# Kernel optimization log

Measured on AMD Instinct MI355X. Metric: run time of the kernel, lower is better.

## Reference

```python
import jax, jax.numpy as jnp
import numpy as np

N = 100000
E = 1600000
D = 128


def setup_inputs() -> dict:
    key = jax.random.key(0)
    ks = jax.random.split(key, 6)
    x = jax.random.normal(ks[0], (N, D), dtype=jnp.float32)
    edge_row = jax.random.randint(ks[1], (E,), 0, N)
    edge_col = jax.random.randint(ks[2], (E,), 0, N)
    edge_val = jax.random.uniform(ks[3], (E,), dtype=jnp.float32)
    # Kaiming-ish init for the MLP weights
    W1 = jax.random.normal(ks[4], (D, D), dtype=jnp.float32) * (1.0 / np.sqrt(D))
    W2 = jax.random.normal(ks[5], (D, D), dtype=jnp.float32) * (1.0 / np.sqrt(D))
    b1 = jnp.zeros((D,), dtype=jnp.float32)
    b2 = jnp.zeros((D,), dtype=jnp.float32)
    eps = jnp.zeros((1,), dtype=jnp.float32)  # GIN eps, init 0
    bias = jnp.zeros((D,), dtype=jnp.float32)
    return {"x": x, "edge_row": edge_row, "edge_col": edge_col, "edge_val": edge_val,
            "W1": W1, "b1": b1, "W2": W2, "b2": b2, "eps": eps, "bias": bias}


def reference(x, edge_row, edge_col, edge_val, W1, b1, W2, b2, eps, bias):
    # sparse adj @ x : out[i] = sum_{edges (i,j)} val * x[j]
    agg = jax.ops.segment_sum(edge_val[:, None] * x[edge_col], edge_row, num_segments=N)
    h = (1.0 + eps) * x + agg                     # eps-scaled residual, [N, D]
    h = jax.nn.relu(h @ W1 + b1)                  # MLP layer 1
    h = jax.nn.relu(h @ W2 + b2)                  # MLP layer 2
    out = jax.nn.relu(h + bias)                   # bias + final relu
    return out
```

## Files before the change

### kernel.cpp

```cpp
#include <hip/hip_runtime.h>
#include <stdint.h>


static constexpr int NN = 100000;
static constexpr int NE = 1600000;
static constexpr int NB = 196;
static constexpr int EPB = 4096;
static constexpr int PB = (NE + EPB - 1) / EPB;

typedef float f32x4 __attribute__((ext_vector_type(4)));
typedef short s16x8 __attribute__((ext_vector_type(8)));

__device__ __forceinline__ uint16_t f2bf(float f) {
  uint32_t u = __float_as_uint(f);
  u += 0x7fffu + ((u >> 16) & 1u);
  return (uint16_t)(u >> 16);
}
__device__ __forceinline__ float2 bf2f(uint32_t w) {
  float2 r;
  r.x = __uint_as_float(w << 16);
  r.y = __uint_as_float(w & 0xffff0000u);
  return r;
}

template <int WIDTH>
__device__ __forceinline__ int* scan_inc(int* s0, int* s1, int tid) {
  int* pin = s0;
  int* pout = s1;
  for (int off = 1; off < WIDTH; off <<= 1) {
    if (tid < WIDTH) pout[tid] = pin[tid] + ((tid >= off) ? pin[tid - off] : 0);
    __syncthreads();
    int* tmp = pin; pin = pout; pout = tmp;
  }
  return pin;
}

__global__ __launch_bounds__(256) void k_cvt(const float* __restrict__ x,
                                             uint32_t* __restrict__ xb, int nq,
                                             int* __restrict__ btot,
                                             int2* __restrict__ es_pad) {
  int i = blockIdx.x * 256 + threadIdx.x;
  if (i < nq) {
    float4 v = ((const float4*)x)[i];
    uint2 o;
    o.x = (uint32_t)f2bf(v.x) | ((uint32_t)f2bf(v.y) << 16);
    o.y = (uint32_t)f2bf(v.z) | ((uint32_t)f2bf(v.w) << 16);
    ((uint2*)xb)[i] = o;
  }
  if (blockIdx.x == 0) {
    int t = threadIdx.x;
    if (t < NB) btot[t] = 0;
    if (t < 8) es_pad[t] = int2{0, 0};
  }
}

__global__ __launch_bounds__(1024) void k_part(const int* __restrict__ erow,
                                               const int* __restrict__ ecol,
                                               const float* __restrict__ eval,
                                               int2* __restrict__ part,
                                               int* __restrict__ runstart,
                                               int* __restrict__ bucket_tot) {
  __shared__ int hist[NB];
  __shared__ int cur[NB];
  __shared__ int s0[256], s1[256];
  __shared__ int2 stage[EPB];
  int t = threadIdx.x;
  int base = blockIdx.x * EPB;
  int cnt = min(EPB, NE - base);

  if (t < NB) hist[t] = 0;
  __syncthreads();

  int pb[4], pk[4], pv[4];
  #pragma unroll
  for (int j = 0; j < 4; ++j) {
    int i = t + j * 1024;
    pb[j] = -1;
    if (i < cnt) {
      int e = base + i;
      int r = erow[e];
      int b = r >> 9;
      pb[j] = b;
      pk[j] = ecol[e] | ((r & 511) << 17);
      pv[j] = __float_as_int(eval[e]);
      atomicAdd(&hist[b], 1);
    }
  }
  __syncthreads();

  if (t < 256) s0[t] = (t < NB) ? hist[t] : 0;
  __syncthreads();
  int* inc = scan_inc<256>(s0, s1, t);

  if (t < NB) {
    int h = hist[t];
    int st = inc[t] - h;
    cur[t] = st;
    runstart[blockIdx.x * (NB + 1) + t] = st;
    atomicAdd(&bucket_tot[t], h);
  }
  if (t == 0) runstart[blockIdx.x * (NB + 1) + NB] = cnt;
  __syncthreads();

  #pragma unroll
  for (int j = 0; j < 4; ++j) {
    if (pb[j] >= 0) {
      int off = atomicAdd(&cur[pb[j]], 1);
      stage[off] = int2{pk[j], pv[j]};
    }
  }
  __syncthreads();

  for (int i = t; i < cnt; i += 1024) part[base + i] = stage[i];
}

__global__ __launch_bounds__(1024) void k_bucket(const int2* __restrict__ part,
                                                 const int* __restrict__ runstart,
                                                 const int* __restrict__ btot,
                                                 int2* __restrict__ es,
                                                 int* __restrict__ rowptr) {
  __shared__ int cum[PB + 1];
  __shared__ int rbas[PB];
  __shared__ int hist[512];
  __shared__ int rps[512];
  __shared__ int cur[512];
  __shared__ int s0[512], s1[512];
  __shared__ int sbase;
  int b = blockIdx.x, t = threadIdx.x;

  int bt = (t < NB) ? btot[t] : 0;
  if (t < 512) s0[t] = (t < 256) ? ((t < NB) ? bt : 0) : 0;
  __syncthreads();
  {
    int* incb = scan_inc<256>(s0, s1, t);
    if (t == b) sbase = incb[b] - bt;
  }
  __syncthreads();
  int base_out = sbase;

  int len = 0;
  if (t < PB) {
    int rs = runstart[t * (NB + 1) + b];
    int re = runstart[t * (NB + 1) + b + 1];
    len = re - rs;
    rbas[t] = t * EPB + rs;
  }
  __syncthreads();
  if (t < 512) s0[t] = (t < PB) ? len : 0;
  __syncthreads();
  int* inc1 = scan_inc<512>(s0, s1, t);
  if (t < PB) cum[t] = inc1[t] - len;
  if (t == 0) cum[PB] = inc1[PB - 1];
  if (t < 512) hist[t] = 0;
  __syncthreads();

  int total = cum[PB];

  int pk[16], pv[16];
  #pragma unroll
  for (int j = 0; j < 16; ++j) {
    int s = t + j * 1024;
    pk[j] = -1;
    if (s < total) {
      int lo = 0, hi = PB;
      while (hi - lo > 1) {
        int mid = (lo + hi) >> 1;
        if (cum[mid] <= s) lo = mid; else hi = mid;
      }
      int2 ev = part[rbas[lo] + (s - cum[lo])];
      pk[j] = ev.x; pv[j] = ev.y;
      atomicAdd(&hist[ev.x >> 17], 1);
    }
  }
  __syncthreads();

  if (t < 512) s0[t] = hist[t];
  __syncthreads();
  int* inc2 = scan_inc<512>(s0, s1, t);
  if (t < 512) {
    int ex = inc2[t] - hist[t];
    rps[t] = ex;
    cur[t] = ex;
  }
  __syncthreads();

  if (t < 512) {
    int row = b * 512 + t;
    if (row <= NN) rowptr[row] = base_out + rps[t];
  }

  #pragma unroll
  for (int j = 0; j < 16; ++j) {
    if (pk[j] >= 0) {
      int rib = pk[j] >> 17;
      int off = atomicAdd(&cur[rib], 1);
      es[base_out + off] = int2{pk[j] & 0x1FFFF, pv[j]};
    }
  }
}

__global__ __launch_bounds__(256) void k_agg(const uint32_t* __restrict__ xb,
                                             const int2* __restrict__ es,
                                             const int* __restrict__ rowptr,
                                             const float* __restrict__ eps,
                                             uint32_t* __restrict__ hb) {
  int wid = (blockIdx.x * 256 + threadIdx.x) >> 6;
  int wave = __builtin_amdgcn_readfirstlane(wid);
  int lane = threadIdx.x & 63;
  float e = 1.0f + eps[0];
  float2 h = bf2f(xb[(size_t)wave * 64 + lane]);
  h.x *= e; h.y *= e;
  int beg = __builtin_amdgcn_readfirstlane(rowptr[wave]);
  int end = __builtin_amdgcn_readfirstlane(rowptr[wave + 1]);
  for (int k = beg; k < end; k += 8) {
    int scol[8]; float sval[8];
    #pragma unroll
    for (int j = 0; j < 8; ++j) {
      int2 ev = es[k + j];
      scol[j] = __builtin_amdgcn_readfirstlane(ev.x);
      int vb = __builtin_amdgcn_readfirstlane(ev.y);
      sval[j] = (k + j < end) ? __int_as_float(vb) : 0.0f;
    }
    uint32_t xw[8];
    #pragma unroll
    for (int j = 0; j < 8; ++j)
      xw[j] = xb[((size_t)scol[j] << 6) + lane];
    #pragma unroll
    for (int j = 0; j < 8; ++j) {
      float2 xv = bf2f(xw[j]);
      h.x = fmaf(sval[j], xv.x, h.x);
      h.y = fmaf(sval[j], xv.y, h.y);
    }
  }
  hb[(size_t)wave * 64 + lane] = (uint32_t)f2bf(h.x) | ((uint32_t)f2bf(h.y) << 16);
}

__global__ __launch_bounds__(256, 3) void k_mlp(const uint16_t* __restrict__ A,
                                                const float* __restrict__ W1,
                                                const float* __restrict__ b1,
                                                const float* __restrict__ W2,
                                                const float* __restrict__ b2,
                                                const float* __restrict__ bias,
                                                float* __restrict__ out, int nrows) {
  __shared__ uint16_t wt[128 * 136];
  __shared__ uint16_t h1[64 * 136];
  int tid = threadIdx.x;

  #pragma unroll 4
  for (int it = 0; it < 64; ++it) {
    int idx = tid + it * 256;
    wt[(idx & 127) * 136 + (idx >> 7)] = f2bf(W1[idx]);
  }
  __syncthreads();

  int wv = tid >> 6, l = tid & 63;
  int m16 = l & 15, qg = l >> 4;
  int r0 = blockIdx.x * 64 + wv * 16;
  int arow = r0 + m16;
  if (arow >= nrows) arow = nrows - 1;

  f32x4 acc[8];
  #pragma unroll
  for (int n0 = 0; n0 < 8; ++n0) acc[n0] = f32x4{0.f, 0.f, 0.f, 0.f};

  #pragma unroll
  for (int k0 = 0; k0 < 128; k0 += 32) {
    s16x8 a = *(const s16x8*)(A + (size_t)arow * 128 + k0 + qg * 8);
    #pragma unroll
    for (int n0 = 0; n0 < 8; ++n0) {
      s16x8 bfr = *(const s16x8*)(&wt[(n0 * 16 + m16) * 136 + k0 + qg * 8]);
      acc[n0] = __builtin_amdgcn_mfma_f32_16x16x32_bf16(a, bfr, acc[n0], 0, 0, 0);
    }
  }

  #pragma unroll
  for (int n0 = 0; n0 < 8; ++n0) {
    int col = n0 * 16 + m16;
    float bb = b1[col];
    #pragma unroll
    for (int j = 0; j < 4; ++j) {
      int lr = wv * 16 + qg * 4 + j;
      h1[lr * 136 + col] = f2bf(fmaxf(acc[n0][j] + bb, 0.0f));
    }
  }
  __syncthreads();

  #pragma unroll 4
  for (int it = 0; it < 64; ++it) {
    int idx = tid + it * 256;
    wt[(idx & 127) * 136 + (idx >> 7)] = f2bf(W2[idx]);
  }
  #pragma unroll
  for (int n0 = 0; n0 < 8; ++n0) acc[n0] = f32x4{0.f, 0.f, 0.f, 0.f};
  __syncthreads();

  #pragma unroll
  for (int k0 = 0; k0 < 128; k0 += 32) {
    s16x8 a = *(const s16x8*)(&h1[(wv * 16 + m16) * 136 + k0 + qg * 8]);
    #pragma unroll
    for (int n0 = 0; n0 < 8; ++n0) {
      s16x8 bfr = *(const s16x8*)(&wt[(n0 * 16 + m16) * 136 + k0 + qg * 8]);
      acc[n0] = __builtin_amdgcn_mfma_f32_16x16x32_bf16(a, bfr, acc[n0], 0, 0, 0);
    }
  }

  #pragma unroll
  for (int n0 = 0; n0 < 8; ++n0) {
    int col = n0 * 16 + m16;
    float bb = b2[col];
    float b3 = bias[col];
    #pragma unroll
    for (int j = 0; j < 4; ++j) {
      int row = r0 + qg * 4 + j;
      if (row < nrows) {
        float v = fmaxf(fmaxf(acc[n0][j] + bb, 0.0f) + b3, 0.0f);
        out[(size_t)row * 128 + col] = v;
      }
    }
  }
}

extern "C" void kernel_launch(void* const* d_in, const int* in_sizes, int n_in,
                              void* d_out, int out_size, void* d_ws, size_t ws_size,
                              hipStream_t stream) {
  const float* x    = (const float*)d_in[0];
  const int*   erow = (const int*)d_in[1];
  const int*   ecol = (const int*)d_in[2];
  const float* eval = (const float*)d_in[3];
  const float* W1   = (const float*)d_in[4];
  const float* b1   = (const float*)d_in[5];
  const float* W2   = (const float*)d_in[6];
  const float* b2   = (const float*)d_in[7];
  const float* eps  = (const float*)d_in[8];
  const float* bias = (const float*)d_in[9];

  char* w = (char*)d_ws;
  size_t off = 0;
  auto take = [&](size_t bytes) -> void* {
    void* p = w + off;
    off = (off + bytes + 255) & ~(size_t)255;
    return p;
  };
  uint32_t* xb     = (uint32_t*)take((size_t)NN * 64 * 4);
  uint32_t* hb     = (uint32_t*)take((size_t)NN * 64 * 4);
  int2*     part   = (int2*)take((size_t)NE * 8);
  int2*     es     = (int2*)take((size_t)(NE + 8) * 8);
  int*      rowptr = (int*)take((size_t)(NN + 1) * 4);
  int*      runst  = (int*)take((size_t)PB * (NB + 1) * 4);
  int*      btot   = (int*)take((size_t)(NB + 1) * 4);
  (void)ws_size;

  k_cvt<<<(NN * 32 + 255) / 256, 256, 0, stream>>>(x, xb, NN * 32, btot, es + NE);
  k_part<<<PB, 1024, 0, stream>>>(erow, ecol, eval, part, runst, btot);
  k_bucket<<<NB, 1024, 0, stream>>>(part, runst, btot, es, rowptr);
  k_agg<<<(NN + 3) / 4, 256, 0, stream>>>(xb, es, rowptr, eps, hb);
  k_mlp<<<(NN + 63) / 64, 256, 0, stream>>>((const uint16_t*)hb, W1, b1, W2, b2,
                                            bias, (float*)d_out, NN);
}
```

Measured before the change: 262.7 us.

## Fuse convert into partition kernel, use shuffle scans, add bucket-base kernel

Merges the bf16 conversion of x into the edge-partition launch as extra blocks. It replaces the global atomic bucket totals with a separate single-block kernel that sums runstart differences and scans them. All shared-memory Hillis-Steele scans become wave-shuffle scans with far fewer barriers, and the aggregation loop is unrolled to 16 edges per batch (es padding grows to 16). The partition buffer now aliases hb to save workspace, which relies on hb being written only after k_bucket has consumed part. The cost is one extra tiny serial launch.

```diff
diff --git a/kernel.cpp b/kernel.cpp
--- a/kernel.cpp
+++ b/kernel.cpp
@@ -7,6 +7,7 @@
 static constexpr int NB = 196;
 static constexpr int EPB = 4096;
 static constexpr int PB = (NE + EPB - 1) / EPB;
+static constexpr int CVB = 3125;
 
 typedef float f32x4 __attribute__((ext_vector_type(4)));
 typedef short s16x8 __attribute__((ext_vector_type(8)));
@@ -23,48 +24,51 @@
   return r;
 }
 
-template <int WIDTH>
-__device__ __forceinline__ int* scan_inc(int* s0, int* s1, int tid) {
-  int* pin = s0;
-  int* pout = s1;
-  for (int off = 1; off < WIDTH; off <<= 1) {
-    if (tid < WIDTH) pout[tid] = pin[tid] + ((tid >= off) ? pin[tid - off] : 0);
-    __syncthreads();
-    int* tmp = pin; pin = pout; pout = tmp;
-  }
-  return pin;
-}
-
-__global__ __launch_bounds__(256) void k_cvt(const float* __restrict__ x,
-                                             uint32_t* __restrict__ xb, int nq,
-                                             int* __restrict__ btot,
-                                             int2* __restrict__ es_pad) {
-  int i = blockIdx.x * 256 + threadIdx.x;
-  if (i < nq) {
+__device__ __forceinline__ int block_scan_inc(int v, int* wsum, int tid) {
+  __syncthreads();
+  int lane = tid & 63, wv = tid >> 6;
+  #pragma unroll
+  for (int off = 1; off < 64; off <<= 1) {
+    int t = __shfl_up(v, off, 64);
+    if (lane >= off) v += t;
+  }
+  if (lane == 63) wsum[wv] = v;
+  __syncthreads();
+  if (wv == 0) {
+    int s = (lane < 16) ? wsum[lane] : 0;
+    #pragma unroll
+    for (int off = 1; off < 16; off <<= 1) {
+      int t = __shfl_up(s, off, 64);
+      if (lane >= off) s += t;
+    }
+    if (lane < 16) wsum[lane] = s;
+  }
+  __syncthreads();
+  if (wv > 0) v += wsum[wv - 1];
+  return v;
+}
+
+__global__ __launch_bounds__(1024) void k_pcvt(const float* __restrict__ x,
+                                               uint32_t* __restrict__ xb,
+                                               const int* __restrict__ erow,
+                                               const int* __restrict__ ecol,
+                                               const float* __restrict__ eval,
+                                               int2* __restrict__ part,
+                                               int* __restrict__ runstart) {
+  int t = threadIdx.x;
+  if (blockIdx.x >= PB) {
+    int i = (blockIdx.x - PB) * 1024 + t;
     float4 v = ((const float4*)x)[i];
     uint2 o;
     o.x = (uint32_t)f2bf(v.x) | ((uint32_t)f2bf(v.y) << 16);
     o.y = (uint32_t)f2bf(v.z) | ((uint32_t)f2bf(v.w) << 16);
     ((uint2*)xb)[i] = o;
-  }
-  if (blockIdx.x == 0) {
-    int t = threadIdx.x;
-    if (t < NB) btot[t] = 0;
-    if (t < 8) es_pad[t] = int2{0, 0};
-  }
-}
-
-__global__ __launch_bounds__(1024) void k_part(const int* __restrict__ erow,
-                                               const int* __restrict__ ecol,
-                                               const float* __restrict__ eval,
-                                               int2* __restrict__ part,
-                                               int* __restrict__ runstart,
-                                               int* __restrict__ bucket_tot) {
+    return;
+  }
   __shared__ int hist[NB];
   __shared__ int cur[NB];
-  __shared__ int s0[256], s1[256];
+  __shared__ int wsum[16];
   __shared__ int2 stage[EPB];
-  int t = threadIdx.x;
   int base = blockIdx.x * EPB;
   int cnt = min(EPB, NE - base);
 
@@ -88,16 +92,12 @@
   }
   __syncthreads();
 
-  if (t < 256) s0[t] = (t < NB) ? hist[t] : 0;
-  __syncthreads();
-  int* inc = scan_inc<256>(s0, s1, t);
-
+  int hv = (t < NB) ? hist[t] : 0;
+  int inc = block_scan_inc(hv, wsum, t);
   if (t < NB) {
-    int h = hist[t];
-    int st = inc[t] - h;
+    int st = inc - hv;
     cur[t] = st;
     runstart[blockIdx.x * (NB + 1) + t] = st;
-    atomicAdd(&bucket_tot[t], h);
   }
   if (t == 0) runstart[blockIdx.x * (NB + 1) + NB] = cnt;
   __syncthreads();
@@ -114,9 +114,30 @@
   for (int i = t; i < cnt; i += 1024) part[base + i] = stage[i];
 }
 
+__global__ __launch_bounds__(1024) void k_bbase(const int* __restrict__ runstart,
+                                                int* __restrict__ bbase,
+                                                int2* __restrict__ es_pad) {
+  __shared__ int psum[4][256];
+  __shared__ int wsum[16];
+  int t = threadIdx.x;
+  int g = t >> 8, b = t & 255;
+  int acc = 0;
+  if (b < NB) {
+    for (int p = g; p < PB; p += 4)
+      acc += runstart[p * (NB + 1) + b + 1] - runstart[p * (NB + 1) + b];
+  }
+  psum[g][b] = acc;
+  __syncthreads();
+  int v = 0;
+  if (g == 0 && b < NB) v = psum[0][b] + psum[1][b] + psum[2][b] + psum[3][b];
+  int inc = block_scan_inc(v, wsum, t);
+  if (g == 0 && b < NB) bbase[b] = inc - v;
+  if (t < 16) es_pad[t] = int2{0, 0};
+}
+
 __global__ __launch_bounds__(1024) void k_bucket(const int2* __restrict__ part,
                                                  const int* __restrict__ runstart,
-                                                 const int* __restrict__ btot,
+                                                 const int* __restrict__ bbase,
                                                  int2* __restrict__ es,
                                                  int* __restrict__ rowptr) {
   __shared__ int cum[PB + 1];
@@ -124,19 +145,9 @@
   __shared__ int hist[512];
   __shared__ int rps[512];
   __shared__ int cur[512];
-  __shared__ int s0[512], s1[512];
-  __shared__ int sbase;
+  __shared__ int wsum[16];
   int b = blockIdx.x, t = threadIdx.x;
-
-  int bt = (t < NB) ? btot[t] : 0;
-  if (t < 512) s0[t] = (t < 256) ? ((t < NB) ? bt : 0) : 0;
-  __syncthreads();
-  {
-    int* incb = scan_inc<256>(s0, s1, t);
-    if (t == b) sbase = incb[b] - bt;
-  }
-  __syncthreads();
-  int base_out = sbase;
+  int base_out = bbase[b];
 
   int len = 0;
   if (t < PB) {
@@ -145,12 +156,9 @@
     len = re - rs;
     rbas[t] = t * EPB + rs;
   }
-  __syncthreads();
-  if (t < 512) s0[t] = (t < PB) ? len : 0;
-  __syncthreads();
-  int* inc1 = scan_inc<512>(s0, s1, t);
-  if (t < PB) cum[t] = inc1[t] - len;
-  if (t == 0) cum[PB] = inc1[PB - 1];
+  int inc1 = block_scan_inc(len, wsum, t);
+  if (t < PB) cum[t] = inc1 - len;
+  if (t == 1023) cum[PB] = inc1;
   if (t < 512) hist[t] = 0;
   __syncthreads();
 
@@ -173,12 +181,10 @@
     }
   }
   __syncthreads();
-
-  if (t < 512) s0[t] = hist[t];
-  __syncthreads();
-  int* inc2 = scan_inc<512>(s0, s1, t);
+  int hv = (t < 512) ? hist[t] : 0;
+  int inc2 = block_scan_inc(hv, wsum, t);
   if (t < 512) {
-    int ex = inc2[t] - hist[t];
+    int ex = inc2 - hv;
     rps[t] = ex;
     cur[t] = ex;
   }
@@ -212,21 +218,21 @@
   h.x *= e; h.y *= e;
   int beg = __builtin_amdgcn_readfirstlane(rowptr[wave]);
   int end = __builtin_amdgcn_readfirstlane(rowptr[wave + 1]);
-  for (int k = beg; k < end; k += 8) {
-    int scol[8]; float sval[8];
-    #pragma unroll
-    for (int j = 0; j < 8; ++j) {
+  for (int k = beg; k < end; k += 16) {
+    int scol[16]; float sval[16];
+    #pragma unroll
+    for (int j = 0; j < 16; ++j) {
       int2 ev = es[k + j];
       scol[j] = __builtin_amdgcn_readfirstlane(ev.x);
       int vb = __builtin_amdgcn_readfirstlane(ev.y);
       sval[j] = (k + j < end) ? __int_as_float(vb) : 0.0f;
     }
-    uint32_t xw[8];
-    #pragma unroll
-    for (int j = 0; j < 8; ++j)
+    uint32_t xw[16];
+    #pragma unroll
+    for (int j = 0; j < 16; ++j)
       xw[j] = xb[((size_t)scol[j] << 6) + lane];
     #pragma unroll
-    for (int j = 0; j < 8; ++j) {
+    for (int j = 0; j < 16; ++j) {
       float2 xv = bf2f(xw[j]);
       h.x = fmaf(sval[j], xv.x, h.x);
       h.y = fmaf(sval[j], xv.y, h.y);
@@ -343,16 +349,16 @@
   };
   uint32_t* xb     = (uint32_t*)take((size_t)NN * 64 * 4);
   uint32_t* hb     = (uint32_t*)take((size_t)NN * 64 * 4);
-  int2*     part   = (int2*)take((size_t)NE * 8);
-  int2*     es     = (int2*)take((size_t)(NE + 8) * 8);
+  int2*     part   = (int2*)hb;
+  int2*     es     = (int2*)take((size_t)(NE + 16) * 8);
   int*      rowptr = (int*)take((size_t)(NN + 1) * 4);
   int*      runst  = (int*)take((size_t)PB * (NB + 1) * 4);
-  int*      btot   = (int*)take((size_t)(NB + 1) * 4);
+  int*      bbase  = (int*)take((size_t)(NB + 1) * 4);
   (void)ws_size;
 
-  k_cvt<<<(NN * 32 + 255) / 256, 256, 0, stream>>>(x, xb, NN * 32, btot, es + NE);
-  k_part<<<PB, 1024, 0, stream>>>(erow, ecol, eval, part, runst, btot);
-  k_bucket<<<NB, 1024, 0, stream>>>(part, runst, btot, es, rowptr);
+  k_pcvt<<<PB + CVB, 1024, 0, stream>>>(x, xb, erow, ecol, eval, part, runst);
+  k_bbase<<<1, 1024, 0, stream>>>(runst, bbase, es + NE);
+  k_bucket<<<NB, 1024, 0, stream>>>(part, runst, bbase, es, rowptr);
   k_agg<<<(NN + 3) / 4, 256, 0, stream>>>(xb, es, rowptr, eps, hb);
   k_mlp<<<(NN + 63) / 64, 256, 0, stream>>>((const uint16_t*)hb, W1, b1, W2, b2,
                                             bias, (float*)d_out, NN);
```

Measured after the change: 270.6 us. +3.0%, slower.
